# Kernel optimization log

Hardware: AMD Instinct MI355X
Metric: run time of the kernel (lower is better)

The kernel has to match this reference:

```python
import jax, jax.numpy as jnp
import numpy as np

V, H, L, NH, MAXS = 32000, 1024, 6, 16, 2048
HD = H // NH
FF = 4 * H
EPS = 1e-5


def _ln(x, s, b):
    m = jnp.mean(x, axis=-1, keepdims=True)
    v = jnp.mean(jnp.square(x - m), axis=-1, keepdims=True)
    return (x - m) * jax.lax.rsqrt(v + EPS) * s + b


def setup_inputs() -> dict:
    key = jax.random.key(0)
    ks = jax.random.split(key, 12)
    s = 0.02
    inp = {
        "input_ids": jax.random.randint(ks[0], (2, 1024), 0, V, dtype=jnp.int64),
        "token_emb": jax.random.normal(ks[1], (V, H), jnp.float32) * s,
        "pos_emb": jax.random.normal(ks[2], (MAXS, H), jnp.float32) * s,
        "ln1_s": jnp.ones((L, H), jnp.float32),
        "ln1_b": jnp.zeros((L, H), jnp.float32),
        "qkv_w": jax.random.normal(ks[3], (L, H, 3 * H), jnp.float32) * s,
        "qkv_b": jnp.zeros((L, 3 * H), jnp.float32),
        "out_w": jax.random.normal(ks[4], (L, H, H), jnp.float32) * s,
        "out_b": jnp.zeros((L, H), jnp.float32),
        "ln2_s": jnp.ones((L, H), jnp.float32),
        "ln2_b": jnp.zeros((L, H), jnp.float32),
        "w1": jax.random.normal(ks[5], (L, H, FF), jnp.float32) * s,
        "b1": jnp.zeros((L, FF), jnp.float32),
        "w2": jax.random.normal(ks[6], (L, FF, H), jnp.float32) * s,
        "b2": jnp.zeros((L, H), jnp.float32),
        "lnf_s": jnp.ones((H,), jnp.float32),
        "lnf_b": jnp.zeros((H,), jnp.float32),
        "lm_w": jax.random.normal(ks[7], (H, V), jnp.float32) * s,
    }
    return inp


def reference(input_ids, token_emb, pos_emb, ln1_s, ln1_b, qkv_w, qkv_b,
              out_w, out_b, ln2_s, ln2_b, w1, b1, w2, b2, lnf_s, lnf_b, lm_w):
    B, S = input_ids.shape
    x = token_emb[input_ids] + pos_emb[:S][None]  # [B,S,H]; dropout = identity (eval)
    for i in range(L):
        # --- attention block ---
        h = _ln(x, ln1_s[i], ln1_b[i])
        qkv = h @ qkv_w[i] + qkv_b[i]                      # [B,S,3H]
        q, k, v = jnp.split(qkv, 3, axis=-1)
        q = q.reshape(B, S, NH, HD)
        k = k.reshape(B, S, NH, HD)
        v = v.reshape(B, S, NH, HD)
        scores = jnp.einsum('bqhd,bkhd->bhqk', q, k) / jnp.sqrt(jnp.float32(HD))
        attn = jax.nn.softmax(scores, axis=-1)             # non-causal, as in source
        o = jnp.einsum('bhqk,bkhd->bqhd', attn, v).reshape(B, S, H)
        x = x + o @ out_w[i] + out_b[i]
        # --- mlp block ---
        h = _ln(x, ln2_s[i], ln2_b[i])
        h = jax.nn.gelu(h @ w1[i] + b1[i], approximate=False)
        x = x + h @ w2[i] + b2[i]
    x = _ln(x, lnf_s, lnf_b)
    logits = x @ lm_w                                      # [B,S,V]
    return logits
```

## Files before the change

kernel.cpp:

```cpp
#include <hip/hip_runtime.h>
#include <hip/hip_bf16.h>
#include <cstdint>
#include <cstddef>

typedef __bf16 bf16;
typedef __attribute__((ext_vector_type(8))) __bf16 bf16x8;
typedef __attribute__((ext_vector_type(4))) __bf16 bf16x4;
typedef __attribute__((ext_vector_type(4))) float f32x4;

__device__ __forceinline__ f32x4 mfma16(bf16x8 a, bf16x8 b, f32x4 c) {
    return __builtin_amdgcn_mfma_f32_16x16x32_bf16(a, b, c, 0, 0, 0);
}

__device__ __forceinline__ void async_copy16(const void* g, void* l) {
    __builtin_amdgcn_global_load_lds((const __attribute__((address_space(1))) void*)g,
                                     (__attribute__((address_space(3))) void*)l,
                                     16, 0, 0);
}

template<int Ncnt> __device__ __forceinline__ void waitv();
template<> __device__ __forceinline__ void waitv<0>() { asm volatile("s_waitcnt vmcnt(0)" ::: "memory"); }
template<> __device__ __forceinline__ void waitv<3>() { asm volatile("s_waitcnt vmcnt(3)" ::: "memory"); }
template<> __device__ __forceinline__ void waitv<4>() { asm volatile("s_waitcnt vmcnt(4)" ::: "memory"); }

__global__ __launch_bounds__(256)
void embed_kernel(const int* __restrict__ ids, const float* __restrict__ te,
                  const float* __restrict__ pe, float* __restrict__ x)
{
    const int row = blockIdx.x;
    const int s = row & 1023;
    const int id = ids[row];
    const f32x4* a = (const f32x4*)(te + (size_t)id * 1024);
    const f32x4* b = (const f32x4*)(pe + (size_t)s * 1024);
    f32x4* o = (f32x4*)(x + (size_t)row * 1024);
    o[threadIdx.x] = a[threadIdx.x] + b[threadIdx.x];
}

__device__ __forceinline__ void ln_body(const float* __restrict__ x, const float* __restrict__ sc,
                                        const float* __restrict__ bi, bf16* __restrict__ out,
                                        int row, int t, float* red)
{
    const f32x4 v = ((const f32x4*)(x + (size_t)row * 1024))[t];
    float s = v[0] + v[1] + v[2] + v[3];
    float q = v[0]*v[0] + v[1]*v[1] + v[2]*v[2] + v[3]*v[3];
    #pragma unroll
    for (int o = 1; o < 64; o <<= 1) { s += __shfl_xor(s, o); q += __shfl_xor(q, o); }
    const int wv = t >> 6, lane = t & 63;
    if (lane == 0) { red[wv] = s; red[4 + wv] = q; }
    __syncthreads();
    s = red[0] + red[1] + red[2] + red[3];
    q = red[4] + red[5] + red[6] + red[7];
    const float mean = s * (1.f / 1024.f);
    const float var  = q * (1.f / 1024.f) - mean * mean;
    const float rstd = rsqrtf(var + 1e-5f);
    const f32x4 scv = ((const f32x4*)sc)[t];
    const f32x4 biv = ((const f32x4*)bi)[t];
    bf16x4 o4;
    #pragma unroll
    for (int j = 0; j < 4; j++) o4[j] = (bf16)((v[j] - mean) * rstd * scv[j] + biv[j]);
    *(bf16x4*)(out + (size_t)row * 1024 + t * 4) = o4;
}

__device__ __forceinline__ void wcvt_body(const float* __restrict__ W, bf16* __restrict__ BT,
                                          int K, int N, int bid, int tidx, float (*tile)[65])
{
    const int nx = N >> 6;
    const int n0 = (bid % nx) << 6, k0 = (bid / nx) << 6;
    const int tx = tidx & 15, ty = tidx >> 4;
    #pragma unroll
    for (int r = 0; r < 4; r++) {
        const f32x4 v = *(const f32x4*)&W[(size_t)(k0 + ty + r*16) * N + n0 + tx*4];
        tile[ty + r*16][tx*4 + 0] = v[0];
        tile[ty + r*16][tx*4 + 1] = v[1];
        tile[ty + r*16][tx*4 + 2] = v[2];
        tile[ty + r*16][tx*4 + 3] = v[3];
    }
    __syncthreads();
    #pragma unroll
    for (int r = 0; r < 4; r++) {
        const int n = ty + r*16;
        bf16x4 o;
        #pragma unroll
        for (int j = 0; j < 4; j++) o[j] = (bf16)tile[tx*4 + j][n];
        *(bf16x4*)&BT[(size_t)(n0 + n) * K + k0 + tx*4] = o;
    }
}

__global__ __launch_bounds__(256)
void front_kernel(const float* __restrict__ x, const float* __restrict__ sc,
                  const float* __restrict__ bi, bf16* __restrict__ out,
                  const float* __restrict__ qkvw0, bf16* __restrict__ wTq,
                  const float* __restrict__ lmw, bf16* __restrict__ wTlm,
                  const float* __restrict__ outw, bf16* __restrict__ wTo_all)
{
    __shared__ float tile[64][65];
    __shared__ float red[8];
    const int bid = blockIdx.x, t = threadIdx.x;
    if (bid < 2048) {
        ln_body(x, sc, bi, out, bid, t, red);
    } else if (bid < 2048 + 768) {
        wcvt_body(qkvw0, wTq, 1024, 3072, bid - 2048, t, tile);
    } else if (bid < 2048 + 768 + 8000) {
        wcvt_body(lmw, wTlm, 1024, 32000, bid - 2816, t, tile);
    } else {
        const int wb = bid - 10816;
        const int l = wb >> 8;
        wcvt_body(outw + (size_t)l * 1024 * 1024, wTo_all + (size_t)l * 1024 * 1024,
                  1024, 1024, wb & 255, t, tile);
    }
}

__global__ __launch_bounds__(256)
void fused_ln_wcvt(const float* __restrict__ x, const float* __restrict__ sc,
                   const float* __restrict__ bi, bf16* __restrict__ out,
                   const float* __restrict__ W1, bf16* __restrict__ BT1, int K1, int N1, int nb1,
                   const float* __restrict__ W2, bf16* __restrict__ BT2, int K2, int N2)
{
    __shared__ float tile[64][65];
    __shared__ float red[8];
    const int bid = blockIdx.x, t = threadIdx.x;
    if (bid < 2048) {
        ln_body(x, sc, bi, out, bid, t, red);
    } else {
        const int wb = bid - 2048;
        if (wb < nb1) wcvt_body(W1, BT1, K1, N1, wb, t, tile);
        else          wcvt_body(W2, BT2, K2, N2, wb - nb1, t, tile);
    }
}

__global__ __launch_bounds__(256)
void vtrans_kernel(const bf16* __restrict__ qkv, bf16* __restrict__ vT)
{
    __shared__ bf16 tile[128][72];
    const int bh = blockIdx.x;
    const int tt = blockIdx.y;
    const int b = bh >> 4, h = bh & 15;
    const bf16* src = qkv + (size_t)b * 1024 * 3072 + 2048 + h * 64;
    const int tid = threadIdx.x;
    #pragma unroll
    for (int i = 0; i < 4; i++) {
        const int c = i * 256 + tid;
        const int tok = c >> 3, dc = c & 7;
        *(bf16x8*)&tile[tok][dc * 8] = *(const bf16x8*)&src[(size_t)(tt*128 + tok) * 3072 + dc * 8];
    }
    __syncthreads();
    #pragma unroll
    for (int i = 0; i < 4; i++) {
        const int c = i * 256 + tid;
        const int d = c & 63, tc = c >> 6;
        bf16x8 v;
        #pragma unroll
        for (int j = 0; j < 8; j++) v[j] = tile[tc*8 + j][d];
        *(bf16x8*)&vT[((size_t)bh * 64 + d) * 1024 + tt*128 + tc*8] = v;
    }
}

__global__ __launch_bounds__(256)
void attn_kernel(const bf16* __restrict__ qkv, const bf16* __restrict__ vT,
                 bf16* __restrict__ attno)
{
    __shared__ __align__(16) bf16 Ksh[128 * 64];
    __shared__ __align__(16) bf16 Vt[64 * 128];
    __shared__ __align__(16) bf16 Plds[4][16][132];

    const int bid = blockIdx.x, tid = threadIdx.x;
    const int b = (bid & 31) >> 4, h = bid & 15;
    const int qb = bid >> 5;
    const int lane = tid & 63, wave = tid >> 6;
    const bf16* base = qkv + (size_t)b * 1024 * 3072;
    const bf16* vbase = vT + (size_t)(b*16 + h) * 64 * 1024;
    const int qrow0 = qb * 64 + wave * 16;
    const int l15 = lane & 15;

    bf16x8 aQ[2];
    {
        const int qr = qrow0 + l15;
        const bf16* qp = base + (size_t)qr * 3072 + h * 64 + ((lane >> 4) << 3);
        aQ[0] = *(const bf16x8*)qp;
        aQ[1] = *(const bf16x8*)(qp + 32);
    }
    float m_i[4] = {-1e30f, -1e30f, -1e30f, -1e30f};
    float l_i[4] = {0.f, 0.f, 0.f, 0.f};
    f32x4 acc[4];
    #pragma unroll
    for (int nb = 0; nb < 4; nb++) acc[nb] = f32x4{0.f, 0.f, 0.f, 0.f};

    const int swzA = (((lane >> 4)     ^ (lane & 7)) << 3);
    const int swzB = (((4 + (lane >> 4)) ^ (lane & 7)) << 3);

    for (int ck = 0; ck < 8; ck++) {
        __syncthreads();
        #pragma unroll
        for (int p = 0; p < 4; p++) {
            const int c = p * 256 + tid;
            const int rw = c >> 3;
            const int kc = (c & 7) ^ (rw & 7);
            async_copy16(base + (size_t)(ck*128 + rw) * 3072 + 1024 + h*64 + kc*8, &Ksh[c * 8]);
        }
        #pragma unroll
        for (int p = 0; p < 4; p++) {
            const int c = p * 256 + tid;
            const int rw = c >> 4;
            const int kc = (c & 15) ^ (rw & 7);
            async_copy16(vbase + (size_t)rw * 1024 + ck*128 + kc*8, &Vt[c * 8]);
        }
        __syncthreads();

        f32x4 sc[8];
        #pragma unroll
        for (int kk = 0; kk < 4; kk++) {
            const int kr0 = (kk*32 + l15) * 64;
            const int kr1 = kr0 + 16*64;
            f32x4 z{0.f, 0.f, 0.f, 0.f};
            z = mfma16(aQ[0], *(const bf16x8*)&Ksh[kr0 + swzA], z);
            z = mfma16(aQ[1], *(const bf16x8*)&Ksh[kr0 + swzB], z);
            sc[2*kk] = z;
            f32x4 z2{0.f, 0.f, 0.f, 0.f};
            z2 = mfma16(aQ[0], *(const bf16x8*)&Ksh[kr1 + swzA], z2);
            z2 = mfma16(aQ[1], *(const bf16x8*)&Ksh[kr1 + swzB], z2);
            sc[2*kk+1] = z2;
        }

        float c[4];
        #pragma unroll
        for (int i = 0; i < 4; i++) {
            float t = sc[0][i];
            #pragma unroll
            for (int e = 1; e < 8; e++) t = fmaxf(t, sc[e][i]);
            #pragma unroll
            for (int o = 1; o < 16; o <<= 1) t = fmaxf(t, __shfl_xor(t, o));
            t *= 0.125f;
            const float mnew = fmaxf(m_i[i], t);
            c[i] = __expf(m_i[i] - mnew);
            float p[8];
            float rs = 0.f;
            #pragma unroll
            for (int e = 0; e < 8; e++) {
                p[e] = __expf(fmaf(sc[e][i], 0.125f, -mnew));
                rs += p[e];
            }
            #pragma unroll
            for (int o = 1; o < 16; o <<= 1) rs += __shfl_xor(rs, o);
            l_i[i] = l_i[i] * c[i] + rs;
            m_i[i] = mnew;
            const int pr = ((lane >> 4) << 2) + i;
            #pragma unroll
            for (int e = 0; e < 8; e++)
                Plds[wave][pr][(e >> 1) * 32 + (e & 1) * 16 + l15] = (bf16)p[e];
        }
        #pragma unroll
        for (int nb = 0; nb < 4; nb++) {
            f32x4 a = acc[nb];
            a[0] *= c[0]; a[1] *= c[1]; a[2] *= c[2]; a[3] *= c[3];
            acc[nb] = a;
        }

        #pragma unroll
        for (int kk = 0; kk < 4; kk++) {
            const bf16x8 aP = *(const bf16x8*)&Plds[wave][l15][kk*32 + ((lane >> 4) << 3)];
            #pragma unroll
            for (int nb = 0; nb < 4; nb++) {
                const int r = nb*16 + l15;
                const int chk = (kk*4 + (lane >> 4)) ^ (r & 7);
                const bf16x8 bV = *(const bf16x8*)&Vt[r*128 + chk*8];
                acc[nb] = mfma16(aP, bV, acc[nb]);
            }
        }
    }
    #pragma unroll
    for (int nb = 0; nb < 4; nb++) {
        #pragma unroll
        for (int i = 0; i < 4; i++) {
            const int row = qrow0 + ((lane >> 4) << 2) + i;
            const float o = acc[nb][i] / l_i[i];
            attno[(size_t)(b*1024 + row) * 1024 + h*64 + nb*16 + l15] = (bf16)o;
        }
    }
}

template<int BM, int BN, int EPI, int KSPLIT>
__global__ __launch_bounds__(512, 2)
void gemm256_kernel(const bf16* __restrict__ A, const bf16* __restrict__ BT,
                    const float* __restrict__ bias, float* __restrict__ resid,
                    bf16* __restrict__ outb, float* __restrict__ outf,
                    int N, int K)
{
    constexpr int MT = 2048 / BM;
    constexpr int FM = BM / 32;
    constexpr int FN = BN / 64;
    constexpr int HM = FM / 2;
    constexpr int LA = BM / 128, LB = BN / 128;
    constexpr int ASUB = BM * 32;
    constexpr int BSUB = BN * 32;
    extern __shared__ __align__(16) char smem_raw[];
    bf16* smem = (bf16*)smem_raw;

    const int nwg = gridDim.x;
    const int q = nwg >> 3, rr = nwg & 7;
    const int xcd = blockIdx.x & 7, ix = blockIdx.x >> 3;
    const int nid = (xcd < rr ? xcd * (q + 1) : rr * (q + 1) + (xcd - rr) * q) + ix;
    const int tiles = nwg / KSPLIT;
    const int ks = nid / tiles;
    const int tile = nid % tiles;
    const int bm = tile % MT, bn = tile / MT;

    const int tid = threadIdx.x, lane = tid & 63, wave = tid >> 6;
    const int wr = wave >> 2, wc = wave & 3;

    f32x4 acc[FM][FN];
    #pragma unroll
    for (int m = 0; m < FM; m++)
        #pragma unroll
        for (int n = 0; n < FN; n++) acc[m][n] = f32x4{0.f, 0.f, 0.f, 0.f};

    const bf16* Abase = A  + (size_t)bm * BM * K;
    const bf16* Bbase = BT + (size_t)bn * BN * K;
    const int Ts = (K >> 6) / KSPLIT;
    const int t0 = ks * Ts;

    const int l15 = lane & 15;
    const int swz = (((lane >> 4) ^ ((l15 >> 1) & 3)) << 3);
    const int arow0 = wr * (BM / 2) + l15;
    const int brow0 = wc * (BN / 4) + l15;

#define ABASE_(p_, ks_) (((p_)*2 + (ks_)) * ASUB)
#define BBASE_(p_, ks_) (4*ASUB + ((p_)*2 + (ks_)) * BSUB)
#define STAGE_A(p_, kt_, ks_) { _Pragma("unroll") for (int i = 0; i < LA; i++) { \
    const int c = tid + i * 512; const int rw = c >> 2; \
    const int kc = (c & 3) ^ ((rw >> 1) & 3); \
    async_copy16(Abase + (size_t)rw * K + (kt_)*64 + (ks_)*32 + kc*8, \
                 &smem[ABASE_(p_, ks_) + c*8]); } }
#define STAGE_B(p_, kt_, ks_) { _Pragma("unroll") for (int i = 0; i < LB; i++) { \
    const int c = tid + i * 512; const int rw = c >> 2; \
    const int kc = (c & 3) ^ ((rw >> 1) & 3); \
    async_copy16(Bbase + (size_t)rw * K + (kt_)*64 + (ks_)*32 + kc*8, \
                 &smem[BBASE_(p_, ks_) + c*8]); } }
#define LOAD_B(p_, ks_) { _Pragma("unroll") for (int n = 0; n < FN; n++) \
    bfv[n] = *(const bf16x8*)&smem[BBASE_(p_, ks_) + (brow0 + n*16)*32 + swz]; }
#define LOAD_A(p_, ks_, mg) { _Pragma("unroll") for (int m = 0; m < HM; m++) \
    af[m] = *(const bf16x8*)&smem[ABASE_(p_, ks_) + (arow0 + ((mg)*HM + m)*16)*32 + swz]; }
#define QUAD(mg) { __builtin_amdgcn_s_setprio(1); \
    _Pragma("unroll") for (int m = 0; m < HM; m++) \
      _Pragma("unroll") for (int n = 0; n < FN; n++) \
        acc[(mg)*HM + m][n] = mfma16(af[m], bfv[n], acc[(mg)*HM + m][n]); \
    __builtin_amdgcn_s_setprio(0); }

    STAGE_A(0, t0, 0); STAGE_B(0, t0, 0); STAGE_A(0, t0, 1); STAGE_B(0, t0, 1);
    waitv<LA + LB>();
    __builtin_amdgcn_s_barrier();

    for (int tl = 0; tl < Ts; tl++) {
        const int b = tl & 1;
        const int kt1 = t0 + tl + 1;
        const bool more = (tl + 1) < Ts;
        bf16x8 af[HM], bfv[FN];
        LOAD_B(b, 0); LOAD_A(b, 0, 0);
        if (more) STAGE_A(b ^ 1, kt1, 0);
        __builtin_amdgcn_s_barrier();
        QUAD(0);
        __builtin_amdgcn_s_barrier();
        LOAD_A(b, 0, 1);
        if (more) STAGE_B(b ^ 1, kt1, 0);
        __builtin_amdgcn_s_barrier();
        QUAD(1);
        if (more) waitv<LA + LB>(); else waitv<0>();
        __builtin_amdgcn_s_barrier();
        LOAD_B(b, 1); LOAD_A(b, 1, 0);
        if (more) STAGE_A(b ^ 1, kt1, 1);
        __builtin_amdgcn_s_barrier();
        QUAD(0);
        __builtin_amdgcn_s_barrier();
        LOAD_A(b, 1, 1);
        if (more) STAGE_B(b ^ 1, kt1, 1);
        __builtin_amdgcn_s_barrier();
        QUAD(1);
        if (more) waitv<LA + LB>();
        __builtin_amdgcn_s_barrier();
    }

    const int er = bm * BM + wr * (BM / 2) + ((lane >> 4) << 2);
    const int ec = bn * BN + wc * (BN / 4) + l15;
    #pragma unroll
    for (int n = 0; n < FN; n++) {
        const int col = ec + n * 16;
        const float bv = (EPI == 3) ? 0.f : ((KSPLIT > 1 && ks != 0) ? 0.f : bias[col]);
        #pragma unroll
        for (int m = 0; m < FM; m++) {
            #pragma unroll
            for (int i = 0; i < 4; i++) {
                const float v = acc[m][n][i] + bv;
                const size_t off = (size_t)(er + m * 16 + i) * N + col;
                if constexpr (EPI == 0) outb[off] = (bf16)v;
                else if constexpr (EPI == 1) {
                    if constexpr (KSPLIT > 1) atomicAdd(&resid[off], v);
                    else resid[off] += v;
                }
                else if constexpr (EPI == 2) {
                    outb[off] = (bf16)(0.5f * v * (1.f + erff(v * 0.70710678118f)));
                } else {
                    outf[off] = v;
                }
            }
        }
    }
#undef ABASE_
#undef BBASE_
#undef STAGE_A
#undef STAGE_B
#undef LOAD_A
#undef LOAD_B
#undef QUAD
}

extern "C" void kernel_launch(void* const* d_in, const int* in_sizes, int n_in,
                              void* d_out, int out_size, void* d_ws, size_t ws_size,
                              hipStream_t stream)
{
    const int*   ids     = (const int*)  d_in[0];
    const float* tok_emb = (const float*)d_in[1];
    const float* pos_emb = (const float*)d_in[2];
    const float* ln1_s   = (const float*)d_in[3];
    const float* ln1_b   = (const float*)d_in[4];
    const float* qkv_w   = (const float*)d_in[5];
    const float* qkv_b   = (const float*)d_in[6];
    const float* out_w   = (const float*)d_in[7];
    const float* out_b   = (const float*)d_in[8];
    const float* ln2_s   = (const float*)d_in[9];
    const float* ln2_b   = (const float*)d_in[10];
    const float* w1      = (const float*)d_in[11];
    const float* b1      = (const float*)d_in[12];
    const float* w2      = (const float*)d_in[13];
    const float* b2      = (const float*)d_in[14];
    const float* lnf_s   = (const float*)d_in[15];
    const float* lnf_b   = (const float*)d_in[16];
    const float* lm_w    = (const float*)d_in[17];

    char* ws = (char*)d_ws;
    float* x    = (float*)ws;  ws += (size_t)2048 * 1024 * 4;
    bf16*  h    = (bf16*)ws;   ws += (size_t)2048 * 1024 * 2;
    bf16*  qkvb = (bf16*)ws;   ws += (size_t)2048 * 3072 * 2;
    bf16*  attno= (bf16*)ws;   ws += (size_t)2048 * 1024 * 2;
    bf16*  vT   = (bf16*)ws;   ws += (size_t)32 * 64 * 1024 * 2;
    bf16*  ff   = (bf16*)ws;   ws += (size_t)2048 * 4096 * 2;
    bf16*  wTq  = (bf16*)ws;   ws += (size_t)3072 * 1024 * 2;
    bf16*  wTo_all = (bf16*)ws; ws += (size_t)6 * 1024 * 1024 * 2;
    bf16*  wT1  = (bf16*)ws;   ws += (size_t)4096 * 1024 * 2;
    bf16*  wT2  = (bf16*)ws;   ws += (size_t)1024 * 4096 * 2;
    bf16*  wTlm = (bf16*)ws;   ws += (size_t)32000 * 1024 * 2;

    embed_kernel<<<2048, 256, 0, stream>>>(ids, tok_emb, pos_emb, x);

    for (int l = 0; l < 6; l++) {
        if (l == 0) {
            front_kernel<<<12352, 256, 0, stream>>>(
                x, ln1_s, ln1_b, h,
                qkv_w, wTq, lm_w, wTlm, out_w, wTo_all);
        } else {
            fused_ln_wcvt<<<2048 + 768, 256, 0, stream>>>(
                x, ln1_s + l*1024, ln1_b + l*1024, h,
                qkv_w + (size_t)l*1024*3072, wTq, 1024, 3072, 768,
                nullptr, nullptr, 0, 0);
        }
        gemm256_kernel<128,256,0,1><<<192, 512, 98304, stream>>>(h, wTq, qkv_b + l*3072, nullptr, qkvb, nullptr, 3072, 1024);
        vtrans_kernel<<<dim3(32, 8), 256, 0, stream>>>(qkvb, vT);
        attn_kernel<<<512, 256, 0, stream>>>(qkvb, vT, attno);
        gemm256_kernel<128,256,1,4><<<256, 512, 98304, stream>>>(attno, wTo_all + (size_t)l*1024*1024, out_b + l*1024, x, nullptr, nullptr, 1024, 1024);
        fused_ln_wcvt<<<2048 + 1024 + 1024, 256, 0, stream>>>(
            x, ln2_s + l*1024, ln2_b + l*1024, h,
            w1 + (size_t)l*1024*4096, wT1, 1024, 4096, 1024,
            w2 + (size_t)l*4096*1024, wT2, 4096, 1024);
        gemm256_kernel<128,256,2,1><<<256, 512, 98304, stream>>>(h, wT1, b1 + l*4096, nullptr, ff, nullptr, 4096, 1024);
        gemm256_kernel<128,256,1,4><<<256, 512, 98304, stream>>>(ff, wT2, b2 + l*1024, x, nullptr, nullptr, 1024, 4096);
    }
    fused_ln_wcvt<<<2048, 256, 0, stream>>>(
        x, lnf_s, lnf_b, h,
        nullptr, nullptr, 0, 0, 0,
        nullptr, nullptr, 0, 0);
    gemm256_kernel<256,256,3,1><<<8*125, 512, 131072, stream>>>(h, wTlm, nullptr, nullptr, nullptr, (float*)d_out, 32000, 1024);
}
```

Baseline: 1.330 ms.

## Hoist all-layer weight conversion into front kernel and fuse V transpose into QKV GEMM

Result: no change. 1.343 ms (+1.0%).

```diff
diff --git a/kernel.cpp b/kernel.cpp
--- a/kernel.cpp
+++ b/kernel.cpp
@@ -83,6 +83,41 @@
         #pragma unroll
         for (int j = 0; j < 4; j++) o[j] = (bf16)tile[tx*4 + j][n];
         *(bf16x4*)&BT[(size_t)(n0 + n) * K + k0 + tx*4] = o;
+    }
+}
+
+__global__ __launch_bounds__(256)
+void front_all_kernel(const float* __restrict__ x, const float* __restrict__ sc,
+                      const float* __restrict__ bi, bf16* __restrict__ out,
+                      const float* __restrict__ qkvw, bf16* __restrict__ wTq_all,
+                      const float* __restrict__ lmw, bf16* __restrict__ wTlm,
+                      const float* __restrict__ outw, bf16* __restrict__ wTo_all,
+                      const float* __restrict__ w1, bf16* __restrict__ wT1_all,
+                      const float* __restrict__ w2, bf16* __restrict__ wT2_all)
+{
+    __shared__ float tile[64][65];
+    __shared__ float red[8];
+    const int bid = blockIdx.x, t = threadIdx.x;
+    if (bid < 2048) {
+        ln_body(x, sc, bi, out, bid, t, red);
+    } else if (bid < 2048 + 4608) {
+        const int wb = bid - 2048, l = wb / 768, sub = wb % 768;
+        wcvt_body(qkvw + (size_t)l * 1024 * 3072, wTq_all + (size_t)l * 3072 * 1024,
+                  1024, 3072, sub, t, tile);
+    } else if (bid < 2048 + 4608 + 8000) {
+        wcvt_body(lmw, wTlm, 1024, 32000, bid - 6656, t, tile);
+    } else if (bid < 2048 + 4608 + 8000 + 1536) {
+        const int wb = bid - 14656, l = wb >> 8;
+        wcvt_body(outw + (size_t)l * 1024 * 1024, wTo_all + (size_t)l * 1024 * 1024,
+                  1024, 1024, wb & 255, t, tile);
+    } else if (bid < 2048 + 4608 + 8000 + 1536 + 6144) {
+        const int wb = bid - 16192, l = wb >> 10;
+        wcvt_body(w1 + (size_t)l * 1024 * 4096, wT1_all + (size_t)l * 4096 * 1024,
+                  1024, 4096, wb & 1023, t, tile);
+    } else {
+        const int wb = bid - 22336, l = wb >> 10;
+        wcvt_body(w2 + (size_t)l * 4096 * 1024, wT2_all + (size_t)l * 1024 * 4096,
+                  4096, 1024, wb & 1023, t, tile);
     }
 }
 
@@ -125,33 +160,6 @@
         const int wb = bid - 2048;
         if (wb < nb1) wcvt_body(W1, BT1, K1, N1, wb, t, tile);
         else          wcvt_body(W2, BT2, K2, N2, wb - nb1, t, tile);
-    }
-}
-
-__global__ __launch_bounds__(256)
-void vtrans_kernel(const bf16* __restrict__ qkv, bf16* __restrict__ vT)
-{
-    __shared__ bf16 tile[128][72];
-    const int bh = blockIdx.x;
-    const int tt = blockIdx.y;
-    const int b = bh >> 4, h = bh & 15;
-    const bf16* src = qkv + (size_t)b * 1024 * 3072 + 2048 + h * 64;
-    const int tid = threadIdx.x;
-    #pragma unroll
-    for (int i = 0; i < 4; i++) {
-        const int c = i * 256 + tid;
-        const int tok = c >> 3, dc = c & 7;
-        *(bf16x8*)&tile[tok][dc * 8] = *(const bf16x8*)&src[(size_t)(tt*128 + tok) * 3072 + dc * 8];
-    }
-    __syncthreads();
-    #pragma unroll
-    for (int i = 0; i < 4; i++) {
-        const int c = i * 256 + tid;
-        const int d = c & 63, tc = c >> 6;
-        bf16x8 v;
-        #pragma unroll
-        for (int j = 0; j < 8; j++) v[j] = tile[tc*8 + j][d];
-        *(bf16x8*)&vT[((size_t)bh * 64 + d) * 1024 + tt*128 + tc*8] = v;
     }
 }
 
@@ -283,7 +291,7 @@
 void gemm256_kernel(const bf16* __restrict__ A, const bf16* __restrict__ BT,
                     const float* __restrict__ bias, float* __restrict__ resid,
                     bf16* __restrict__ outb, float* __restrict__ outf,
-                    int N, int K)
+                    bf16* __restrict__ vt, int N, int K)
 {
     constexpr int MT = 2048 / BM;
     constexpr int FM = BM / 32;
@@ -386,19 +394,34 @@
         const float bv = (EPI == 3) ? 0.f : ((KSPLIT > 1 && ks != 0) ? 0.f : bias[col]);
         #pragma unroll
         for (int m = 0; m < FM; m++) {
-            #pragma unroll
-            for (int i = 0; i < 4; i++) {
-                const float v = acc[m][n][i] + bv;
-                const size_t off = (size_t)(er + m * 16 + i) * N + col;
-                if constexpr (EPI == 0) outb[off] = (bf16)v;
-                else if constexpr (EPI == 1) {
-                    if constexpr (KSPLIT > 1) atomicAdd(&resid[off], v);
-                    else resid[off] += v;
+            const int row0 = er + m * 16;
+            if constexpr (EPI == 4) {
+                if (col < 2048) {
+                    #pragma unroll
+                    for (int i = 0; i < 4; i++)
+                        outb[(size_t)(row0 + i) * N + col] = (bf16)(acc[m][n][i] + bv);
+                } else {
+                    bf16x4 o4;
+                    #pragma unroll
+                    for (int i = 0; i < 4; i++) o4[i] = (bf16)(acc[m][n][i] + bv);
+                    const int b_ = row0 >> 10, tok = row0 & 1023;
+                    *(bf16x4*)&vt[((size_t)(b_ * 1024 + (col - 2048))) * 1024 + tok] = o4;
                 }
-                else if constexpr (EPI == 2) {
-                    outb[off] = (bf16)(0.5f * v * (1.f + erff(v * 0.70710678118f)));
-                } else {
-                    outf[off] = v;
+            } else {
+                #pragma unroll
+                for (int i = 0; i < 4; i++) {
+                    const float v = acc[m][n][i] + bv;
+                    const size_t off = (size_t)(row0 + i) * N + col;
+                    if constexpr (EPI == 0) outb[off] = (bf16)v;
+                    else if constexpr (EPI == 1) {
+                        if constexpr (KSPLIT > 1) atomicAdd(&resid[off], v);
+                        else resid[off] += v;
+                    }
+                    else if constexpr (EPI == 2) {
+                        outb[off] = (bf16)(0.5f * v * (1.f + erff(v * 0.70710678118f)));
+                    } else {
+                        outf[off] = v;
+                    }
                 }
             }
         }
@@ -442,39 +465,81 @@
     bf16*  attno= (bf16*)ws;   ws += (size_t)2048 * 1024 * 2;
     bf16*  vT   = (bf16*)ws;   ws += (size_t)32 * 64 * 1024 * 2;
     bf16*  ff   = (bf16*)ws;   ws += (size_t)2048 * 4096 * 2;
-    bf16*  wTq  = (bf16*)ws;   ws += (size_t)3072 * 1024 * 2;
     bf16*  wTo_all = (bf16*)ws; ws += (size_t)6 * 1024 * 1024 * 2;
-    bf16*  wT1  = (bf16*)ws;   ws += (size_t)4096 * 1024 * 2;
-    bf16*  wT2  = (bf16*)ws;   ws += (size_t)1024 * 4096 * 2;
     bf16*  wTlm = (bf16*)ws;   ws += (size_t)32000 * 1024 * 2;
 
+    const size_t base_used = (size_t)(ws - (char*)d_ws);
+    const size_t hoist_need = base_used + ((size_t)6*3072*1024 + (size_t)6*4096*1024 + (size_t)6*1024*4096) * 2;
+    const size_t small_need = base_used + ((size_t)3072*1024 + (size_t)4096*1024 + (size_t)1024*4096) * 2;
+    const bool hoist = (ws_size >= hoist_need);
+    (void)small_need;
+
+    bf16* wTq_all = (bf16*)ws;
+    bf16* wT1_all;
+    bf16* wT2_all;
+    if (hoist) {
+        ws += (size_t)6 * 3072 * 1024 * 2;
+        wT1_all = (bf16*)ws; ws += (size_t)6 * 4096 * 1024 * 2;
+        wT2_all = (bf16*)ws;
+    } else {
+        ws += (size_t)3072 * 1024 * 2;
+        wT1_all = (bf16*)ws; ws += (size_t)4096 * 1024 * 2;
+        wT2_all = (bf16*)ws;
+    }
+
     embed_kernel<<<2048, 256, 0, stream>>>(ids, tok_emb, pos_emb, x);
 
     for (int l = 0; l < 6; l++) {
+        const size_t lq = hoist ? (size_t)l * 3072 * 1024 : 0;
+        const size_t l1 = hoist ? (size_t)l * 4096 * 1024 : 0;
+        const size_t l2 = hoist ? (size_t)l * 1024 * 4096 : 0;
         if (l == 0) {
-            front_kernel<<<12352, 256, 0, stream>>>(
-                x, ln1_s, ln1_b, h,
-                qkv_w, wTq, lm_w, wTlm, out_w, wTo_all);
+            if (hoist) {
+                front_all_kernel<<<28480, 256, 0, stream>>>(
+                    x, ln1_s, ln1_b, h,
+                    qkv_w, wTq_all, lm_w, wTlm, out_w, wTo_all,
+                    w1, wT1_all, w2, wT2_all);
+            } else {
+                front_kernel<<<12352, 256, 0, stream>>>(
+                    x, ln1_s, ln1_b, h,
+                    qkv_w, wTq_all, lm_w, wTlm, out_w, wTo_all);
+            }
         } else {
-            fused_ln_wcvt<<<2048 + 768, 256, 0, stream>>>(
-                x, ln1_s + l*1024, ln1_b + l*1024, h,
-                qkv_w + (size_t)l*1024*3072, wTq, 1024, 3072, 768,
-                nullptr, nullptr, 0, 0);
-        }
-        gemm256_kernel<128,256,0,1><<<192, 512, 98304, stream>>>(h, wTq, qkv_b + l*3072, nullptr, qkvb, nullptr, 3072, 1024);
-        vtrans_kernel<<<dim3(32, 8), 256, 0, stream>>>(qkvb, vT);
+            if (hoist) {
+                fused_ln_wcvt<<<2048, 256, 0, stream>>>(
+                    x, ln1_s + l*1024, ln1_b + l*1024, h,
+                    nullptr, nullptr, 0, 0, 0, nullptr, nullptr, 0, 0);
+            } else {
+                fused_ln_wcvt<<<2048 + 768, 256, 0, stream>>>(
+                    x, ln1_s + l*1024, ln1_b + l*1024, h,
+                    qkv_w + (size_t)l*1024*3072, wTq_all, 1024, 3072, 768,
+                    nullptr, nullptr, 0, 0);
+            }
+        }
+        gemm256_kernel<128,256,4,1><<<192, 512, 98304, stream>>>(
+            h, wTq_all + lq, qkv_b + l*3072, nullptr, qkvb, nullptr, vT, 3072, 1024);
         attn_kernel<<<512, 256, 0, stream>>>(qkvb, vT, attno);
-        gemm256_kernel<128,256,1,4><<<256, 512, 98304, stream>>>(attno, wTo_all + (size_t)l*1024*1024, out_b + l*1024, x, nullptr, nullptr, 1024, 1024);
-        fused_ln_wcvt<<<2048 + 1024 + 1024, 256, 0, stream>>>(
-            x, ln2_s + l*1024, ln2_b + l*1024, h,
-            w1 + (size_t)l*1024*4096, wT1, 1024, 4096, 1024,
-            w2 + (size_t)l*4096*1024, wT2, 4096, 1024);
-        gemm256_kernel<128,256,2,1><<<256, 512, 98304, stream>>>(h, wT1, b1 + l*4096, nullptr, ff, nullptr, 4096, 1024);
-        gemm256_kernel<128,256,1,4><<<256, 512, 98304, stream>>>(ff, wT2, b2 + l*1024, x, nullptr, nullptr, 1024, 4096);
+        gemm256_kernel<128,256,1,4><<<256, 512, 98304, stream>>>(
+            attno, wTo_all + (size_t)l*1024*1024, out_b + l*1024, x, nullptr, nullptr, nullptr, 1024, 1024);
+        if (hoist) {
+            fused_ln_wcvt<<<2048, 256, 0, stream>>>(
+                x, ln2_s + l*1024, ln2_b + l*1024, h,
+                nullptr, nullptr, 0, 0, 0, nullptr, nullptr, 0, 0);
+        } else {
+            fused_ln_wcvt<<<2048 + 1024 + 1024, 256, 0, stream>>>(
+                x, ln2_s + l*1024, ln2_b + l*1024, h,
+                w1 + (size_t)l*1024*4096, wT1_all, 1024, 4096, 1024,
+                w2 + (size_t)l*4096*1024, wT2_all, 4096, 1024);
+        }
+        gemm256_kernel<128,256,2,1><<<256, 512, 98304, stream>>>(
+            h, wT1_all + l1, b1 + l*4096, nullptr, ff, nullptr, nullptr, 4096, 1024);
+        gemm256_kernel<128,256,1,4><<<256, 512, 98304, stream>>>(
+            ff, wT2_all + l2, b2 + l*1024, x, nullptr, nullptr, nullptr, 1024, 4096);
     }
     fused_ln_wcvt<<<2048, 256, 0, stream>>>(
         x, lnf_s, lnf_b, h,
         nullptr, nullptr, 0, 0, 0,
         nullptr, nullptr, 0, 0);
-    gemm256_kernel<256,256,3,1><<<8*125, 512, 131072, stream>>>(h, wTlm, nullptr, nullptr, nullptr, (float*)d_out, 32000, 1024);
-}
+    gemm256_kernel<256,256,3,1><<<8*125, 512, 131072, stream>>>(
+        h, wTlm, nullptr, nullptr, nullptr, (float*)d_out, nullptr, 32000, 1024);
+}
```

## Fuse V transpose into QKV GEMM epilogue and retile QKV GEMM to 128x192

Applied to the files above, without the earlier changes.

Measured after the change: 1.304 ms. 2.0% less time.

```diff
diff --git a/kernel.cpp b/kernel.cpp
--- a/kernel.cpp
+++ b/kernel.cpp
@@ -20,8 +20,15 @@
 
 template<int Ncnt> __device__ __forceinline__ void waitv();
 template<> __device__ __forceinline__ void waitv<0>() { asm volatile("s_waitcnt vmcnt(0)" ::: "memory"); }
+template<> __device__ __forceinline__ void waitv<2>() { asm volatile("s_waitcnt vmcnt(2)" ::: "memory"); }
 template<> __device__ __forceinline__ void waitv<3>() { asm volatile("s_waitcnt vmcnt(3)" ::: "memory"); }
 template<> __device__ __forceinline__ void waitv<4>() { asm volatile("s_waitcnt vmcnt(4)" ::: "memory"); }
+
+__device__ __forceinline__ void wait_g(int n) {
+    if (n == 2) waitv<2>();
+    else if (n == 3) waitv<3>();
+    else waitv<4>();
+}
 
 __global__ __launch_bounds__(256)
 void embed_kernel(const int* __restrict__ ids, const float* __restrict__ te,
@@ -129,33 +136,6 @@
 }
 
 __global__ __launch_bounds__(256)
-void vtrans_kernel(const bf16* __restrict__ qkv, bf16* __restrict__ vT)
-{
-    __shared__ bf16 tile[128][72];
-    const int bh = blockIdx.x;
-    const int tt = blockIdx.y;
-    const int b = bh >> 4, h = bh & 15;
-    const bf16* src = qkv + (size_t)b * 1024 * 3072 + 2048 + h * 64;
-    const int tid = threadIdx.x;
-    #pragma unroll
-    for (int i = 0; i < 4; i++) {
-        const int c = i * 256 + tid;
-        const int tok = c >> 3, dc = c & 7;
-        *(bf16x8*)&tile[tok][dc * 8] = *(const bf16x8*)&src[(size_t)(tt*128 + tok) * 3072 + dc * 8];
-    }
-    __syncthreads();
-    #pragma unroll
-    for (int i = 0; i < 4; i++) {
-        const int c = i * 256 + tid;
-        const int d = c & 63, tc = c >> 6;
-        bf16x8 v;
-        #pragma unroll
-        for (int j = 0; j < 8; j++) v[j] = tile[tc*8 + j][d];
-        *(bf16x8*)&vT[((size_t)bh * 64 + d) * 1024 + tt*128 + tc*8] = v;
-    }
-}
-
-__global__ __launch_bounds__(256)
 void attn_kernel(const bf16* __restrict__ qkv, const bf16* __restrict__ vT,
                  bf16* __restrict__ attno)
 {
@@ -283,13 +263,16 @@
 void gemm256_kernel(const bf16* __restrict__ A, const bf16* __restrict__ BT,
                     const float* __restrict__ bias, float* __restrict__ resid,
                     bf16* __restrict__ outb, float* __restrict__ outf,
-                    int N, int K)
+                    bf16* __restrict__ vt, int N, int K)
 {
     constexpr int MT = 2048 / BM;
     constexpr int FM = BM / 32;
     constexpr int FN = BN / 64;
     constexpr int HM = FM / 2;
-    constexpr int LA = BM / 128, LB = BN / 128;
+    constexpr int ACH = BM * 4;
+    constexpr int BCH = BN * 4;
+    constexpr int LA = (ACH + 511) >> 9;
+    constexpr int LB = (BCH + 511) >> 9;
     constexpr int ASUB = BM * 32;
     constexpr int BSUB = BN * 32;
     extern __shared__ __align__(16) char smem_raw[];
@@ -307,6 +290,10 @@
     const int tid = threadIdx.x, lane = tid & 63, wave = tid >> 6;
     const int wr = wave >> 2, wc = wave & 3;
 
+    const int myB = ((BCH & 511) == 0) ? (BCH >> 9)
+                    : ((tid < (BCH & 511)) ? (BCH >> 9) + 1 : (BCH >> 9));
+    const int wcount = LA + myB;
+
     f32x4 acc[FM][FN];
     #pragma unroll
     for (int m = 0; m < FM; m++)
@@ -326,15 +313,19 @@
 #define ABASE_(p_, ks_) (((p_)*2 + (ks_)) * ASUB)
 #define BBASE_(p_, ks_) (4*ASUB + ((p_)*2 + (ks_)) * BSUB)
 #define STAGE_A(p_, kt_, ks_) { _Pragma("unroll") for (int i = 0; i < LA; i++) { \
-    const int c = tid + i * 512; const int rw = c >> 2; \
-    const int kc = (c & 3) ^ ((rw >> 1) & 3); \
-    async_copy16(Abase + (size_t)rw * K + (kt_)*64 + (ks_)*32 + kc*8, \
-                 &smem[ABASE_(p_, ks_) + c*8]); } }
+    const int c = tid + i * 512; \
+    if ((ACH & 511) == 0 || c < ACH) { \
+      const int rw = c >> 2; \
+      const int kc = (c & 3) ^ ((rw >> 1) & 3); \
+      async_copy16(Abase + (size_t)rw * K + (kt_)*64 + (ks_)*32 + kc*8, \
+                   &smem[ABASE_(p_, ks_) + c*8]); } } }
 #define STAGE_B(p_, kt_, ks_) { _Pragma("unroll") for (int i = 0; i < LB; i++) { \
-    const int c = tid + i * 512; const int rw = c >> 2; \
-    const int kc = (c & 3) ^ ((rw >> 1) & 3); \
-    async_copy16(Bbase + (size_t)rw * K + (kt_)*64 + (ks_)*32 + kc*8, \
-                 &smem[BBASE_(p_, ks_) + c*8]); } }
+    const int c = tid + i * 512; \
+    if ((BCH & 511) == 0 || c < BCH) { \
+      const int rw = c >> 2; \
+      const int kc = (c & 3) ^ ((rw >> 1) & 3); \
+      async_copy16(Bbase + (size_t)rw * K + (kt_)*64 + (ks_)*32 + kc*8, \
+                   &smem[BBASE_(p_, ks_) + c*8]); } } }
 #define LOAD_B(p_, ks_) { _Pragma("unroll") for (int n = 0; n < FN; n++) \
     bfv[n] = *(const bf16x8*)&smem[BBASE_(p_, ks_) + (brow0 + n*16)*32 + swz]; }
 #define LOAD_A(p_, ks_, mg) { _Pragma("unroll") for (int m = 0; m < HM; m++) \
@@ -346,7 +337,7 @@
     __builtin_amdgcn_s_setprio(0); }
 
     STAGE_A(0, t0, 0); STAGE_B(0, t0, 0); STAGE_A(0, t0, 1); STAGE_B(0, t0, 1);
-    waitv<LA + LB>();
+    wait_g(wcount);
     __builtin_amdgcn_s_barrier();
 
     for (int tl = 0; tl < Ts; tl++) {
@@ -363,7 +354,7 @@
         if (more) STAGE_B(b ^ 1, kt1, 0);
         __builtin_amdgcn_s_barrier();
         QUAD(1);
-        if (more) waitv<LA + LB>(); else waitv<0>();
+        if (more) wait_g(wcount); else waitv<0>();
         __builtin_amdgcn_s_barrier();
         LOAD_B(b, 1); LOAD_A(b, 1, 0);
         if (more) STAGE_A(b ^ 1, kt1, 1);
@@ -374,7 +365,7 @@
         if (more) STAGE_B(b ^ 1, kt1, 1);
         __builtin_amdgcn_s_barrier();
         QUAD(1);
-        if (more) waitv<LA + LB>();
+        if (more) wait_g(wcount);
         __builtin_amdgcn_s_barrier();
     }
 
@@ -386,19 +377,34 @@
         const float bv = (EPI == 3) ? 0.f : ((KSPLIT > 1 && ks != 0) ? 0.f : bias[col]);
         #pragma unroll
         for (int m = 0; m < FM; m++) {
-            #pragma unroll
-            for (int i = 0; i < 4; i++) {
-                const float v = acc[m][n][i] + bv;
-                const size_t off = (size_t)(er + m * 16 + i) * N + col;
-                if constexpr (EPI == 0) outb[off] = (bf16)v;
-                else if constexpr (EPI == 1) {
-                    if constexpr (KSPLIT > 1) atomicAdd(&resid[off], v);
-                    else resid[off] += v;
+            const int row0 = er + m * 16;
+            if constexpr (EPI == 4) {
+                if (col < 2048) {
+                    #pragma unroll
+                    for (int i = 0; i < 4; i++)
+                        outb[(size_t)(row0 + i) * N + col] = (bf16)(acc[m][n][i] + bv);
+                } else {
+                    bf16x4 o4;
+                    #pragma unroll
+                    for (int i = 0; i < 4; i++) o4[i] = (bf16)(acc[m][n][i] + bv);
+                    const int b_ = row0 >> 10, tok = row0 & 1023;
+                    *(bf16x4*)&vt[((size_t)(b_ * 1024 + (col - 2048))) * 1024 + tok] = o4;
                 }
-                else if constexpr (EPI == 2) {
-                    outb[off] = (bf16)(0.5f * v * (1.f + erff(v * 0.70710678118f)));
-                } else {
-                    outf[off] = v;
+            } else {
+                #pragma unroll
+                for (int i = 0; i < 4; i++) {
+                    const float v = acc[m][n][i] + bv;
+                    const size_t off = (size_t)(row0 + i) * N + col;
+                    if constexpr (EPI == 0) outb[off] = (bf16)v;
+                    else if constexpr (EPI == 1) {
+                        if constexpr (KSPLIT > 1) atomicAdd(&resid[off], v);
+                        else resid[off] += v;
+                    }
+                    else if constexpr (EPI == 2) {
+                        outb[off] = (bf16)(0.5f * v * (1.f + erff(v * 0.70710678118f)));
+                    } else {
+                        outf[off] = v;
+                    }
                 }
             }
         }
@@ -461,20 +467,24 @@
                 qkv_w + (size_t)l*1024*3072, wTq, 1024, 3072, 768,
                 nullptr, nullptr, 0, 0);
         }
-        gemm256_kernel<128,256,0,1><<<192, 512, 98304, stream>>>(h, wTq, qkv_b + l*3072, nullptr, qkvb, nullptr, 3072, 1024);
-        vtrans_kernel<<<dim3(32, 8), 256, 0, stream>>>(qkvb, vT);
+        gemm256_kernel<128,192,4,1><<<256, 512, 81920, stream>>>(
+            h, wTq, qkv_b + l*3072, nullptr, qkvb, nullptr, vT, 3072, 1024);
         attn_kernel<<<512, 256, 0, stream>>>(qkvb, vT, attno);
-        gemm256_kernel<128,256,1,4><<<256, 512, 98304, stream>>>(attno, wTo_all + (size_t)l*1024*1024, out_b + l*1024, x, nullptr, nullptr, 1024, 1024);
+        gemm256_kernel<128,256,1,4><<<256, 512, 98304, stream>>>(
+            attno, wTo_all + (size_t)l*1024*1024, out_b + l*1024, x, nullptr, nullptr, nullptr, 1024, 1024);
         fused_ln_wcvt<<<2048 + 1024 + 1024, 256, 0, stream>>>(
             x, ln2_s + l*1024, ln2_b + l*1024, h,
             w1 + (size_t)l*1024*4096, wT1, 1024, 4096, 1024,
             w2 + (size_t)l*4096*1024, wT2, 4096, 1024);
-        gemm256_kernel<128,256,2,1><<<256, 512, 98304, stream>>>(h, wT1, b1 + l*4096, nullptr, ff, nullptr, 4096, 1024);
-        gemm256_kernel<128,256,1,4><<<256, 512, 98304, stream>>>(ff, wT2, b2 + l*1024, x, nullptr, nullptr, 1024, 4096);
+        gemm256_kernel<128,256,2,1><<<256, 512, 98304, stream>>>(
+            h, wT1, b1 + l*4096, nullptr, ff, nullptr, nullptr, 4096, 1024);
+        gemm256_kernel<128,256,1,4><<<256, 512, 98304, stream>>>(
+            ff, wT2, b2 + l*1024, x, nullptr, nullptr, nullptr, 1024, 4096);
     }
     fused_ln_wcvt<<<2048, 256, 0, stream>>>(
         x, lnf_s, lnf_b, h,
         nullptr, nullptr, 0, 0, 0,
         nullptr, nullptr, 0, 0);
-    gemm256_kernel<256,256,3,1><<<8*125, 512, 131072, stream>>>(h, wTlm, nullptr, nullptr, nullptr, (float*)d_out, 32000, 1024);
-}
+    gemm256_kernel<256,256,3,1><<<8*125, 512, 131072, stream>>>(
+        h, wTlm, nullptr, nullptr, nullptr, (float*)d_out, nullptr, 32000, 1024);
+}
```
